# Optimization experiments

Measured on AMD Instinct MI355X. Metric: run time of the kernel, lower is better.

The kernel has to match this reference:

```python
import jax, jax.numpy as jnp
import numpy as np

B, S, D, H, DK, DFF = 4, 1024, 1024, 16, 64, 4096
EPS = 1e-5


def layer_norm(x, g, b):
    m = jnp.mean(x, axis=-1, keepdims=True)
    v = jnp.var(x, axis=-1, keepdims=True)
    return (x - m) * jax.lax.rsqrt(v + EPS) * g + b


def setup_inputs() -> dict:
    key = jax.random.key(0)
    ks = jax.random.split(key, 12)
    sc = 0.02
    return {
        "x":    jax.random.normal(ks[0], (B, S, D), jnp.float32),
        # per-head Q/K/V projections, stacked over heads: [H, D, DK]
        "Wq":   jax.random.normal(ks[1], (H, D, DK), jnp.float32) * sc,
        "bq":   jnp.zeros((H, DK), jnp.float32),
        "Wk":   jax.random.normal(ks[2], (H, D, DK), jnp.float32) * sc,
        "bk":   jnp.zeros((H, DK), jnp.float32),
        "Wv":   jax.random.normal(ks[3], (H, D, DK), jnp.float32) * sc,
        "bv":   jnp.zeros((H, DK), jnp.float32),
        # output projection: [H*DK, D]
        "Wo":   jax.random.normal(ks[4], (H * DK, D), jnp.float32) * sc,
        "bo":   jnp.zeros((D,), jnp.float32),
        # FFN
        "W1":   jax.random.normal(ks[5], (D, DFF), jnp.float32) * sc,
        "b1":   jnp.zeros((DFF,), jnp.float32),
        "W2":   jax.random.normal(ks[6], (DFF, D), jnp.float32) * sc,
        "b2":   jnp.zeros((D,), jnp.float32),
        # LayerNorms
        "g1":   jnp.ones((D,), jnp.float32),
        "be1":  jnp.zeros((D,), jnp.float32),
        "g2":   jnp.ones((D,), jnp.float32),
        "be2":  jnp.zeros((D,), jnp.float32),
    }


def reference(x, Wq, bq, Wk, bk, Wv, bv, Wo, bo, W1, b1, W2, b2, g1, be1, g2, be2):
    # batched multi-head attention (original loops per head; math identical)
    q = jnp.einsum("bsd,hdk->bhsk", x, Wq) + bq[None, :, None, :]
    k = jnp.einsum("bsd,hdk->bhsk", x, Wk) + bk[None, :, None, :]
    v = jnp.einsum("bsd,hdk->bhsk", x, Wv) + bv[None, :, None, :]
    scale = 1.0 / jnp.sqrt(jnp.asarray(DK, x.dtype))
    scores = jnp.einsum("bhsk,bhtk->bhst", q * scale, k)
    attn = jax.nn.softmax(scores, axis=-1)  # dropout = eval-mode identity
    o = jnp.einsum("bhst,bhtk->bhsk", attn, v)
    # torch.cat over heads along dim 2 -> [B, S, H*DK]
    o = jnp.transpose(o, (0, 2, 1, 3)).reshape(B, S, H * DK)
    att = o @ Wo + bo
    # post-attn: residual of LayerNorm(att)
    x = x + layer_norm(att, g1, be1)
    # FFN
    pos = jax.nn.relu(x @ W1 + b1) @ W2 + b2
    x = x + layer_norm(pos, g2, be2)
    return x
```

## Files before the change

### kernel.cpp

```cpp
#include <hip/hip_runtime.h>
#include <hip/hip_bf16.h>
#include <hip/hip_fp16.h>

typedef unsigned short u16;
typedef short bf16x8_t __attribute__((ext_vector_type(8)));
typedef float f32x4_t  __attribute__((ext_vector_type(4)));

__device__ __forceinline__ u16 f2bf(float f) {
    __hip_bfloat16 h = __float2bfloat16(f);
    union { __hip_bfloat16 b; u16 u; } cv; cv.b = h; return cv.u;
}

__device__ __forceinline__ void g2l16(const void* g, void* l) {
    __builtin_amdgcn_global_load_lds(
        (const __attribute__((address_space(1))) unsigned int*)g,
        (__attribute__((address_space(3))) unsigned int*)l, 16, 0, 0);
}

__global__ __launch_bounds__(256)
void k_prep(const float* __restrict__ x, u16* __restrict__ Xb,
            const float* __restrict__ Wq, const float* __restrict__ Wk,
            const float* __restrict__ Wv, u16* __restrict__ Wqkvt,
            const float* __restrict__ Wo, const float* __restrict__ W1,
            const float* __restrict__ W2, u16* __restrict__ Wot,
            u16* __restrict__ W1t, u16* __restrict__ W2t)
{
    int id = blockIdx.x;
    if (id < 4096) {
        int i = id * 256 + threadIdx.x;
        float4 f = ((const float4*)x)[i];
        ushort4 o;
        o.x = f2bf(f.x); o.y = f2bf(f.y); o.z = f2bf(f.z); o.w = f2bf(f.w);
        ((ushort4*)Xb)[i] = o;
        return;
    }
    id -= 4096;
    const float* in; u16* out; int R, C, r0, c0;
    if (id < 768) {
        int zx = id >> 8, hy = (id >> 4) & 15, tx = id & 15;
        in  = (zx == 0 ? Wq : (zx == 1 ? Wk : Wv)) + (size_t)hy * 65536;
        out = Wqkvt + ((size_t)zx * 1024 + hy * 64) * 1024;
        R = 1024; C = 64; r0 = tx * 64; c0 = 0;
    } else {
        id -= 768;
        int tx, ty;
        if (id < 256)       { in = Wo; out = Wot; R = 1024; C = 1024; tx = id & 15; ty = id >> 4; }
        else if (id < 1280) { id -= 256; in = W1; out = W1t; R = 1024; C = 4096; tx = id & 63; ty = id >> 6; }
        else                { id -= 1280; in = W2; out = W2t; R = 4096; C = 1024; tx = id & 15; ty = id >> 4; }
        r0 = ty * 64; c0 = tx * 64;
    }
    __shared__ float t[64][65];
    int lc = threadIdx.x & 63, lr = threadIdx.x >> 6;
#pragma unroll
    for (int p = 0; p < 16; ++p) {
        int rr = p * 4 + lr;
        t[rr][lc] = in[(size_t)(r0 + rr) * C + c0 + lc];
    }
    __syncthreads();
#pragma unroll
    for (int p = 0; p < 16; ++p) {
        int cc = p * 4 + lr;
        out[(size_t)(c0 + cc) * R + r0 + lc] = f2bf(t[lc][cc]);
    }
}

__global__ __launch_bounds__(256)
void k_vt(const u16* __restrict__ V, u16* __restrict__ VT) {
    __shared__ u16 t[64 * 72];
    int bh = blockIdx.y, s0 = blockIdx.x * 64;
    const u16* Vp = V + (size_t)bh * 65536;
    u16* Tp = VT + (size_t)bh * 65536;
    int tid = threadIdx.x;
    int r = tid >> 3, c = (tid & 7) * 8;
    *(uint4*)&t[r * 72 + c]        = *(const uint4*)&Vp[(size_t)(s0 + r) * 64 + c];
    *(uint4*)&t[(r + 32) * 72 + c] = *(const uint4*)&Vp[(size_t)(s0 + r + 32) * 64 + c];
    __syncthreads();
    int d = tid >> 2, sl0 = (tid & 3) * 16;
    uint4 outv[2];
    u16* ov = (u16*)outv;
#pragma unroll
    for (int j = 0; j < 16; ++j) ov[j] = t[(sl0 + j) * 72 + d];
    *(uint4*)&Tp[(size_t)d * 1024 + s0 + sl0]     = outv[0];
    *(uint4*)&Tp[(size_t)d * 1024 + s0 + sl0 + 8] = outv[1];
}

__global__ __launch_bounds__(256, 4)
void k_gemm_bt(const u16* __restrict__ A, const u16* __restrict__ Bt,
               void* __restrict__ out, int M, int N, int K, int kchunk)
{
    __shared__ __align__(16) u16 As[2 * 128 * 32];
    __shared__ __align__(16) u16 Bs[2 * 128 * 32];
    int tid = threadIdx.x;
    int wave = tid >> 6, lane = tid & 63;

    int nx = gridDim.x, nwg = nx * gridDim.y;
    int f  = blockIdx.x + nx * blockIdx.y;
    int f2 = (f & 7) * (nwg >> 3) + (f >> 3);
    int bx = f2 % nx, by = f2 / nx;
    int row0 = by * 128, col0 = bx * 128;

    int z = blockIdx.z;
    int kbeg = z * kchunk;

    int lrow = lane >> 2, lcol = (lane & 3) * 8;
    const u16* pA0 = A  + (size_t)(row0 + wave * 16 + lrow) * K + kbeg + lcol;
    const u16* pA1 = pA0 + (size_t)64 * K;
    const u16* pB0 = Bt + (size_t)(col0 + wave * 16 + lrow) * K + kbeg + lcol;
    const u16* pB1 = pB0 + (size_t)64 * K;
    u16* lA0 = &As[wave * 512];
    u16* lA1 = &As[2048 + wave * 512];
    u16* lB0 = &Bs[wave * 512];
    u16* lB1 = &Bs[2048 + wave * 512];

    int wm = (wave >> 1) * 64, wn = (wave & 1) * 64;
    int quad = lane >> 4, l16 = lane & 15;

    f32x4_t acc[4][4];
#pragma unroll
    for (int i = 0; i < 4; i++)
#pragma unroll
        for (int j = 0; j < 4; j++) acc[i][j] = f32x4_t{0.f, 0.f, 0.f, 0.f};

    for (int kk = 0; kk < kchunk; kk += 64) {
        __syncthreads();
        g2l16(pA0, lA0);      g2l16(pA1, lA1);
        g2l16(pA0 + 32, lA0 + 4096); g2l16(pA1 + 32, lA1 + 4096);
        g2l16(pB0, lB0);      g2l16(pB1, lB1);
        g2l16(pB0 + 32, lB0 + 4096); g2l16(pB1 + 32, lB1 + 4096);
        pA0 += 64; pA1 += 64; pB0 += 64; pB1 += 64;
        __syncthreads();

#pragma unroll
        for (int s = 0; s < 2; ++s) {
            const u16* as = &As[s * 4096];
            const u16* bs = &Bs[s * 4096];
            bf16x8_t a[4], b[4];
#pragma unroll
            for (int i = 0; i < 4; ++i)
                a[i] = *(const bf16x8_t*)&as[(wm + i * 16 + l16) * 32 + quad * 8];
#pragma unroll
            for (int j = 0; j < 4; ++j)
                b[j] = *(const bf16x8_t*)&bs[(wn + j * 16 + l16) * 32 + quad * 8];
#pragma unroll
            for (int i = 0; i < 4; ++i)
#pragma unroll
                for (int j = 0; j < 4; ++j)
                    acc[i][j] = __builtin_amdgcn_mfma_f32_16x16x32_bf16(a[i], b[j], acc[i][j], 0, 0, 0);
        }
    }

#pragma unroll
    for (int i = 0; i < 4; ++i)
#pragma unroll
        for (int j = 0; j < 4; ++j)
#pragma unroll
            for (int r = 0; r < 4; ++r) {
                int row = row0 + wm + i * 16 + quad * 4 + r;
                int col = col0 + wn + j * 16 + l16;
                ((__half*)out)[(size_t)z * M * N + (size_t)row * N + col] =
                    __float2half(acc[i][j][r]);
            }
}

template<int EPI>
__global__ __launch_bounds__(512, 4)
void k_gemm_bt2(const u16* __restrict__ A, const u16* __restrict__ Bt,
                const float* __restrict__ bias0, const float* __restrict__ bias1,
                const float* __restrict__ bias2, void* __restrict__ out,
                int M, int N, int K)
{
    __shared__ __align__(16) u16 As[2 * 256 * 32];
    __shared__ __align__(16) u16 Bs[2 * 128 * 32];
    int tid = threadIdx.x;
    int wave = tid >> 6, lane = tid & 63;
    int row0 = blockIdx.y * 256, col0 = blockIdx.x * 128;

    int lrow = lane >> 2, lcol = (lane & 3) * 8;
    const u16* pA0 = A  + (size_t)(row0 + wave * 16 + lrow) * K + lcol;
    const u16* pA1 = pA0 + (size_t)128 * K;
    const u16* pB0 = Bt + (size_t)(col0 + wave * 16 + lrow) * K + lcol;
    u16* lA0 = &As[wave * 512];
    u16* lA1 = &As[4096 + wave * 512];
    u16* lB0 = &Bs[wave * 512];

    int wm = (wave >> 1) * 64, wn = (wave & 1) * 64;
    int quad = lane >> 4, l16 = lane & 15;

    f32x4_t acc[4][4];
#pragma unroll
    for (int i = 0; i < 4; i++)
#pragma unroll
        for (int j = 0; j < 4; j++) acc[i][j] = f32x4_t{0.f, 0.f, 0.f, 0.f};

    for (int kk = 0; kk < K; kk += 64) {
        __syncthreads();
        g2l16(pA0, lA0);           g2l16(pA1, lA1);
        g2l16(pA0 + 32, lA0 + 8192); g2l16(pA1 + 32, lA1 + 8192);
        g2l16(pB0, lB0);           g2l16(pB0 + 32, lB0 + 4096);
        pA0 += 64; pA1 += 64; pB0 += 64;
        __syncthreads();

#pragma unroll
        for (int s = 0; s < 2; ++s) {
            const u16* as = &As[s * 8192];
            const u16* bs = &Bs[s * 4096];
            bf16x8_t a[4], b[4];
#pragma unroll
            for (int i = 0; i < 4; ++i)
                a[i] = *(const bf16x8_t*)&as[(wm + i * 16 + l16) * 32 + quad * 8];
#pragma unroll
            for (int j = 0; j < 4; ++j)
                b[j] = *(const bf16x8_t*)&bs[(wn + j * 16 + l16) * 32 + quad * 8];
#pragma unroll
            for (int i = 0; i < 4; ++i)
#pragma unroll
                for (int j = 0; j < 4; ++j)
                    acc[i][j] = __builtin_amdgcn_mfma_f32_16x16x32_bf16(a[i], b[j], acc[i][j], 0, 0, 0);
        }
    }

#pragma unroll
    for (int i = 0; i < 4; ++i)
#pragma unroll
        for (int j = 0; j < 4; ++j)
#pragma unroll
            for (int r = 0; r < 4; ++r) {
                int row = row0 + wm + i * 16 + quad * 4 + r;
                int col = col0 + wn + j * 16 + l16;
                float v = acc[i][j][r];
                if (EPI == 1) {
                    ((u16*)out)[(size_t)row * N + col] = f2bf(fmaxf(v + bias0[col], 0.f));
                } else {
                    int proj = col >> 10, within = col & 1023;
                    const float* bp = proj == 0 ? bias0 : (proj == 1 ? bias1 : bias2);
                    v += bp[within];
                    if (proj == 0) v *= 0.18033688f;
                    int h = within >> 6, kq = within & 63;
                    int b_ = row >> 10, s_ = row & 1023;
                    size_t bh = (size_t)((b_ << 4) + h);
                    ((u16*)out)[(size_t)proj * 4194304 + bh * 65536 + (s_ << 6) + kq] = f2bf(v);
                }
            }
}

__global__ __launch_bounds__(512, 4)
void k_attn(const u16* __restrict__ Qg, const u16* __restrict__ Kg,
            const u16* __restrict__ VTg, u16* __restrict__ Og)
{
    __shared__ __align__(16) u16 Ks[64 * 64];
    __shared__ __align__(16) u16 Vs[64 * 64];
    __shared__ __align__(16) u16 Ps[128 * 64];

    int tid = threadIdx.x, wave = tid >> 6, lane = tid & 63;
    int quad = lane >> 4, l16 = lane & 15;

    int f  = blockIdx.x + gridDim.x * blockIdx.y;
    int f2 = (f & 7) * ((gridDim.x * gridDim.y) >> 3) + (f >> 3);
    int bh = f2 >> 3;
    int q0 = (f2 & 7) * 128;
    int wrow = wave * 16;

    const u16* Qp  = Qg  + (size_t)bh * 65536;
    const u16* Kp  = Kg  + (size_t)bh * 65536;
    const u16* VTp = VTg + (size_t)bh * 65536;

    int arow_g = q0 + wrow + l16;
    bf16x8_t aq0 = *(const bf16x8_t*)&Qp[(size_t)arow_g * 64 + quad * 8];
    bf16x8_t aq1 = *(const bf16x8_t*)&Qp[(size_t)arow_g * 64 + 32 + quad * 8];

    int srow = tid >> 3, scb = tid & 7;
    uint4 kreg = *(const uint4*)&Kp[(size_t)srow * 64 + scb * 8];
    uint4 vreg = *(const uint4*)&VTp[(size_t)srow * 1024 + scb * 8];
    u16* kdst = &Ks[srow * 64 + ((scb ^ (srow & 7)) * 8)];
    u16* vdst = &Vs[srow * 64 + ((scb ^ (srow & 7)) * 8)];

    f32x4_t o[4], lsum;
#pragma unroll
    for (int nt = 0; nt < 4; ++nt) o[nt] = f32x4_t{0.f, 0.f, 0.f, 0.f};
    lsum = f32x4_t{0.f, 0.f, 0.f, 0.f};

    bf16x8_t ones;
#pragma unroll
    for (int j = 0; j < 8; ++j) ones[j] = (short)0x3F80;

    int a7 = l16 & 7;

    for (int kv0 = 0; kv0 < 1024; kv0 += 64) {
        __syncthreads();
        *(uint4*)kdst = kreg;
        *(uint4*)vdst = vreg;
        __syncthreads();
        if (kv0 < 960) {
            kreg = *(const uint4*)&Kp[(size_t)(kv0 + 64 + srow) * 64 + scb * 8];
            vreg = *(const uint4*)&VTp[(size_t)srow * 1024 + kv0 + 64 + scb * 8];
        }

        f32x4_t s[4];
#pragma unroll
        for (int nt = 0; nt < 4; ++nt) {
            int brow = nt * 16 + l16;
            bf16x8_t bk0 = *(const bf16x8_t*)&Ks[brow * 64 + ((quad ^ a7) * 8)];
            bf16x8_t bk1 = *(const bf16x8_t*)&Ks[brow * 64 + (((4 + quad) ^ a7) * 8)];
            s[nt] = __builtin_amdgcn_mfma_f32_16x16x32_bf16(aq0, bk0, f32x4_t{0.f,0.f,0.f,0.f}, 0, 0, 0);
            s[nt] = __builtin_amdgcn_mfma_f32_16x16x32_bf16(aq1, bk1, s[nt], 0, 0, 0);
        }

#pragma unroll
        for (int nt = 0; nt < 4; ++nt) {
            int pcb = nt * 2 + (l16 >> 3);
#pragma unroll
            for (int r = 0; r < 4; ++r) {
                float p = exp2f(s[nt][r]);
                int pr = wrow + quad * 4 + r;
                Ps[pr * 64 + ((pcb ^ (pr & 7)) * 8) + (l16 & 7)] = f2bf(p);
            }
        }

        int arow = wrow + l16;
        bf16x8_t ap0 = *(const bf16x8_t*)&Ps[arow * 64 + ((quad ^ a7) * 8)];
        bf16x8_t ap1 = *(const bf16x8_t*)&Ps[arow * 64 + (((4 + quad) ^ a7) * 8)];
#pragma unroll
        for (int nt = 0; nt < 4; ++nt) {
            int vrow = nt * 16 + l16;
            bf16x8_t bv0 = *(const bf16x8_t*)&Vs[vrow * 64 + ((quad ^ a7) * 8)];
            bf16x8_t bv1 = *(const bf16x8_t*)&Vs[vrow * 64 + (((4 + quad) ^ a7) * 8)];
            o[nt] = __builtin_amdgcn_mfma_f32_16x16x32_bf16(ap0, bv0, o[nt], 0, 0, 0);
            o[nt] = __builtin_amdgcn_mfma_f32_16x16x32_bf16(ap1, bv1, o[nt], 0, 0, 0);
        }
        lsum = __builtin_amdgcn_mfma_f32_16x16x32_bf16(ap0, ones, lsum, 0, 0, 0);
        lsum = __builtin_amdgcn_mfma_f32_16x16x32_bf16(ap1, ones, lsum, 0, 0, 0);
    }

    int b = bh >> 4, h = bh & 15;
    float invl[4];
#pragma unroll
    for (int r = 0; r < 4; ++r) invl[r] = 1.f / lsum[r];
#pragma unroll
    for (int nt = 0; nt < 4; ++nt)
#pragma unroll
        for (int r = 0; r < 4; ++r) {
            int srow2 = q0 + wrow + quad * 4 + r;
            Og[(size_t)(b * 1024 + srow2) * 1024 + (h << 6) + nt * 16 + l16] = f2bf(o[nt][r] * invl[r]);
        }
}

template<int MODE, int NP>
__global__ __launch_bounds__(256)
void k_ln2(const __half* __restrict__ p, const float* __restrict__ bias,
           const float* __restrict__ residf, const u16* __restrict__ residb,
           const float* __restrict__ g, const float* __restrict__ be,
           float* __restrict__ out, u16* __restrict__ outb)
{
    int row = blockIdx.x, tid = threadIdx.x;
    size_t base = (size_t)row * 1024;
    float xv[4]; float s = 0.f, sq = 0.f;
#pragma unroll
    for (int i = 0; i < 4; i++) {
        int c = tid + i * 256;
        float t = bias[c];
#pragma unroll
        for (int z = 0; z < NP; ++z) t += __half2float(p[(size_t)z * 4194304 + base + c]);
        xv[i] = t;
        s += t; sq += t * t;
    }
#pragma unroll
    for (int off = 32; off; off >>= 1) { s += __shfl_down(s, off); sq += __shfl_down(sq, off); }
    __shared__ float ss[4], ssq[4];
    int wv = tid >> 6;
    if ((tid & 63) == 0) { ss[wv] = s; ssq[wv] = sq; }
    __syncthreads();
    s  = ss[0] + ss[1] + ss[2] + ss[3];
    sq = ssq[0] + ssq[1] + ssq[2] + ssq[3];
    float mean = s * (1.f / 1024.f);
    float var  = sq * (1.f / 1024.f) - mean * mean;
    float rstd = rsqrtf(var + 1e-5f);
#pragma unroll
    for (int i = 0; i < 4; i++) {
        int c = tid + i * 256;
        float rv;
        if (MODE == 0) rv = residf[base + c];
        else {
            union { u16 u[2]; unsigned int w; float f; } cv;
            cv.w = (unsigned int)residb[base + c] << 16;
            rv = cv.f;
        }
        float y = rv + (xv[i] - mean) * rstd * g[c] + be[c];
        if (MODE == 0) outb[base + c] = f2bf(y);
        else           out[base + c] = y;
    }
}

extern "C" void kernel_launch(void* const* d_in, const int* in_sizes, int n_in,
                              void* d_out, int out_size, void* d_ws, size_t ws_size,
                              hipStream_t stream) {
    const float* x   = (const float*)d_in[0];
    const float* Wq  = (const float*)d_in[1];
    const float* bq  = (const float*)d_in[2];
    const float* Wk  = (const float*)d_in[3];
    const float* bk  = (const float*)d_in[4];
    const float* Wv  = (const float*)d_in[5];
    const float* bv  = (const float*)d_in[6];
    const float* Wo  = (const float*)d_in[7];
    const float* bo  = (const float*)d_in[8];
    const float* W1  = (const float*)d_in[9];
    const float* b1  = (const float*)d_in[10];
    const float* W2  = (const float*)d_in[11];
    const float* b2  = (const float*)d_in[12];
    const float* g1  = (const float*)d_in[13];
    const float* be1 = (const float*)d_in[14];
    const float* g2  = (const float*)d_in[15];
    const float* be2 = (const float*)d_in[16];
    float* out = (float*)d_out;

    char* w = (char*)d_ws;
    u16*    Xb    = (u16*)(w);
    u16*    VTb   = (u16*)(w);
    u16*    Wqkvt = (u16*)(w + 8388608);
    u16*    Wot   = (u16*)(w + 14680064);
    u16*    W1t   = (u16*)(w + 16777216);
    u16*    W2t   = (u16*)(w + 25165824);
    u16*    Qb    = (u16*)(w + 33554432);
    u16*    Kb    = (u16*)(w + 41943040);
    u16*    Vb    = (u16*)(w + 50331648);
    u16*    Oc    = (u16*)(w + 58720256);
    __half* part4 = (__half*)(w + 33554432);
    __half* part2 = (__half*)(w + 67108864);
    u16*    x1b   = (u16*)(w + 117440512);
    u16*    hb    = (u16*)(w + 125829120);

    k_prep<<<7168, 256, 0, stream>>>(x, Xb, Wq, Wk, Wv, Wqkvt, Wo, W1, W2, Wot, W1t, W2t);

    k_gemm_bt2<2><<<dim3(24, 16), 512, 0, stream>>>(Xb, Wqkvt, bq, bk, bv, Qb, 4096, 3072, 1024);

    k_vt<<<dim3(16, 64), 256, 0, stream>>>(Vb, VTb);

    k_attn<<<dim3(8, 64), 512, 0, stream>>>(Qb, Kb, VTb, Oc);

    k_gemm_bt<<<dim3(8, 32, 2), 256, 0, stream>>>(Oc, Wot, part2, 4096, 1024, 1024, 512);

    k_ln2<0, 2><<<4096, 256, 0, stream>>>(part2, bo, x, nullptr, g1, be1, nullptr, x1b);

    k_gemm_bt2<1><<<dim3(32, 16), 512, 0, stream>>>(x1b, W1t, b1, nullptr, nullptr, hb, 4096, 4096, 1024);

    k_gemm_bt<<<dim3(8, 32, 4), 256, 0, stream>>>(hb, W2t, part4, 4096, 1024, 4096, 1024);

    k_ln2<1, 4><<<4096, 256, 0, stream>>>(part4, b2, nullptr, x1b, g2, be2, out, nullptr);
}
```

Measured before the change: 308.4 us.

## Add 256x256-tile ping-pong GEMM kernel for both FFN matmuls

Introduces a new bf16 MFMA GEMM with 256x256 block tiles, 8 waves each computing 128x64, double-buffered LDS filled by direct global-to-LDS loads, and interleaved quarter-tile MFMA phases with setprio and barriers to overlap loads with compute. It replaces the previous kernels for the W1 (bias+ReLU epilogue) and W2 (split-K fp16 partials) FFN GEMMs. The aim is more data reuse per LDS load and better overlap of memory traffic with math. In exchange it uses 128KB of LDS per block and launches fewer workgroups, which lowers occupancy and leaves fewer blocks to spread across the CUs.

```diff
diff --git a/kernel.cpp b/kernel.cpp
--- a/kernel.cpp
+++ b/kernel.cpp
@@ -239,6 +239,151 @@
                     int b_ = row >> 10, s_ = row & 1023;
                     size_t bh = (size_t)((b_ << 4) + h);
                     ((u16*)out)[(size_t)proj * 4194304 + bh * 65536 + (s_ << 6) + kq] = f2bf(v);
+                }
+            }
+}
+
+template<int EPI>
+__global__ __launch_bounds__(512, 2)
+void k_gemm8p(const u16* __restrict__ A, const u16* __restrict__ Bt,
+              const float* __restrict__ bias0, void* __restrict__ out,
+              int M, int N, int K, int kchunk)
+{
+    __shared__ __align__(16) u16 As[2][16384];
+    __shared__ __align__(16) u16 Bs[2][16384];
+
+    const int tid = threadIdx.x;
+    const int wave = tid >> 6, lane = tid & 63;
+    const int quad = lane >> 4, l16 = lane & 15;
+    const int wm = (wave >> 2) * 128;
+    const int wn = (wave & 3) * 64;
+
+    int nx = gridDim.x, nwg = nx * gridDim.y;
+    int f  = blockIdx.x + nx * blockIdx.y;
+    int f2 = (f & 7) * (nwg >> 3) + (f >> 3);
+    int row0 = (f2 / nx) * 256, col0 = (f2 % nx) * 256;
+    int z = blockIdx.z, kbeg = z * kchunk;
+    int nk = kchunk >> 6;
+
+    const int rr0 = tid >> 3, cg = tid & 7;
+    const int xc = (cg ^ (rr0 & 7)) * 8;
+    const u16* Ag = A  + (size_t)(row0 + rr0) * K + kbeg + xc;
+    const u16* Bg = Bt + (size_t)(col0 + rr0) * K + kbeg + xc;
+    const int ldst = tid * 8;
+
+#define STA(bsel, h, kt) do { \
+    const u16* _s = Ag + (size_t)(h) * 128 * K + (size_t)(kt) * 64; \
+    g2l16(_s, &As[bsel][(h) * 8192 + ldst]); \
+    g2l16(_s + (size_t)64 * K, &As[bsel][(h) * 8192 + 4096 + ldst]); } while (0)
+#define STB(bsel, h, kt) do { \
+    const u16* _s = Bg + (size_t)(h) * 128 * K + (size_t)(kt) * 64; \
+    g2l16(_s, &Bs[bsel][(h) * 8192 + ldst]); \
+    g2l16(_s + (size_t)64 * K, &Bs[bsel][(h) * 8192 + 4096 + ldst]); } while (0)
+
+#define RDA(b, mi, ks) (*(const bf16x8_t*)&As[b][(wm + (mi) * 16 + l16) * 64 + ((((ks) * 4 + quad) ^ (l16 & 7)) * 8)])
+#define RDB(b, nj, ks) (*(const bf16x8_t*)&Bs[b][(wn + (nj) * 16 + l16) * 64 + ((((ks) * 4 + quad) ^ (l16 & 7)) * 8)])
+
+    f32x4_t acc[8][4];
+#pragma unroll
+    for (int i = 0; i < 8; ++i)
+#pragma unroll
+        for (int j = 0; j < 4; ++j) acc[i][j] = f32x4_t{0.f, 0.f, 0.f, 0.f};
+
+    bf16x8_t av0[4][2], av1[4][2], bv0[2][2], bv1[2][2];
+
+    STA(0, 0, 0); STA(0, 1, 0); STB(0, 0, 0); STB(0, 1, 0);
+    if (nk > 1) {
+        STB(1, 0, 1);
+        asm volatile("s_waitcnt vmcnt(2)" ::: "memory");
+    } else {
+        asm volatile("s_waitcnt vmcnt(0)" ::: "memory");
+    }
+    __builtin_amdgcn_s_barrier();
+#pragma unroll
+    for (int i = 0; i < 4; ++i) { av0[i][0] = RDA(0, i, 0); av0[i][1] = RDA(0, i, 1); }
+#pragma unroll
+    for (int j = 0; j < 2; ++j) { bv0[j][0] = RDB(0, j, 0); bv0[j][1] = RDB(0, j, 1); }
+    __builtin_amdgcn_sched_barrier(0);
+
+    for (int t = 0; t < nk; ++t) {
+        int b = t & 1, bn = b ^ 1;
+        if (t + 1 < nk) STB(bn, 1, t + 1);
+#pragma unroll
+        for (int j = 0; j < 2; ++j) { bv1[j][0] = RDB(b, 2 + j, 0); bv1[j][1] = RDB(b, 2 + j, 1); }
+        __builtin_amdgcn_sched_barrier(0);
+        __builtin_amdgcn_s_setprio(1);
+#pragma unroll
+        for (int i = 0; i < 4; ++i)
+#pragma unroll
+            for (int j = 0; j < 2; ++j) {
+                acc[i][j] = __builtin_amdgcn_mfma_f32_16x16x32_bf16(av0[i][0], bv0[j][0], acc[i][j], 0, 0, 0);
+                acc[i][j] = __builtin_amdgcn_mfma_f32_16x16x32_bf16(av0[i][1], bv0[j][1], acc[i][j], 0, 0, 0);
+            }
+        __builtin_amdgcn_s_setprio(0);
+        __builtin_amdgcn_s_barrier();
+        if (t + 1 < nk) { STA(bn, 0, t + 1); STA(bn, 1, t + 1); }
+#pragma unroll
+        for (int i = 0; i < 4; ++i) { av1[i][0] = RDA(b, 4 + i, 0); av1[i][1] = RDA(b, 4 + i, 1); }
+        __builtin_amdgcn_sched_barrier(0);
+        __builtin_amdgcn_s_setprio(1);
+#pragma unroll
+        for (int i = 0; i < 4; ++i)
+#pragma unroll
+            for (int j = 0; j < 2; ++j) {
+                acc[i][2 + j] = __builtin_amdgcn_mfma_f32_16x16x32_bf16(av0[i][0], bv1[j][0], acc[i][2 + j], 0, 0, 0);
+                acc[i][2 + j] = __builtin_amdgcn_mfma_f32_16x16x32_bf16(av0[i][1], bv1[j][1], acc[i][2 + j], 0, 0, 0);
+            }
+        __builtin_amdgcn_s_setprio(0);
+        __builtin_amdgcn_s_barrier();
+        __builtin_amdgcn_s_setprio(1);
+#pragma unroll
+        for (int i = 0; i < 4; ++i)
+#pragma unroll
+            for (int j = 0; j < 2; ++j) {
+                acc[4 + i][j] = __builtin_amdgcn_mfma_f32_16x16x32_bf16(av1[i][0], bv0[j][0], acc[4 + i][j], 0, 0, 0);
+                acc[4 + i][j] = __builtin_amdgcn_mfma_f32_16x16x32_bf16(av1[i][1], bv0[j][1], acc[4 + i][j], 0, 0, 0);
+            }
+        __builtin_amdgcn_s_setprio(0);
+        __builtin_amdgcn_s_barrier();
+        asm volatile("s_waitcnt vmcnt(0)" ::: "memory");
+        if (t + 2 < nk) STB(b, 0, t + 2);
+        __builtin_amdgcn_s_barrier();
+        if (t + 1 < nk) {
+#pragma unroll
+            for (int i = 0; i < 4; ++i) { av0[i][0] = RDA(bn, i, 0); av0[i][1] = RDA(bn, i, 1); }
+#pragma unroll
+            for (int j = 0; j < 2; ++j) { bv0[j][0] = RDB(bn, j, 0); bv0[j][1] = RDB(bn, j, 1); }
+            __builtin_amdgcn_sched_barrier(0);
+        }
+        __builtin_amdgcn_s_setprio(1);
+#pragma unroll
+        for (int i = 0; i < 4; ++i)
+#pragma unroll
+            for (int j = 0; j < 2; ++j) {
+                acc[4 + i][2 + j] = __builtin_amdgcn_mfma_f32_16x16x32_bf16(av1[i][0], bv1[j][0], acc[4 + i][2 + j], 0, 0, 0);
+                acc[4 + i][2 + j] = __builtin_amdgcn_mfma_f32_16x16x32_bf16(av1[i][1], bv1[j][1], acc[4 + i][2 + j], 0, 0, 0);
+            }
+        __builtin_amdgcn_s_setprio(0);
+        __builtin_amdgcn_s_barrier();
+    }
+#undef STA
+#undef STB
+#undef RDA
+#undef RDB
+
+#pragma unroll
+    for (int mi = 0; mi < 8; ++mi)
+#pragma unroll
+        for (int nj = 0; nj < 4; ++nj)
+#pragma unroll
+            for (int r = 0; r < 4; ++r) {
+                int row = row0 + wm + mi * 16 + quad * 4 + r;
+                int col = col0 + wn + nj * 16 + l16;
+                float v = acc[mi][nj][r];
+                if (EPI == 0) {
+                    ((__half*)out)[(size_t)z * M * N + (size_t)row * N + col] = __float2half(v);
+                } else {
+                    ((u16*)out)[(size_t)row * N + col] = f2bf(fmaxf(v + bias0[col], 0.f));
                 }
             }
 }
@@ -440,9 +585,9 @@
 
     k_ln2<0, 2><<<4096, 256, 0, stream>>>(part2, bo, x, nullptr, g1, be1, nullptr, x1b);
 
-    k_gemm_bt2<1><<<dim3(32, 16), 512, 0, stream>>>(x1b, W1t, b1, nullptr, nullptr, hb, 4096, 4096, 1024);
-
-    k_gemm_bt<<<dim3(8, 32, 4), 256, 0, stream>>>(hb, W2t, part4, 4096, 1024, 4096, 1024);
+    k_gemm8p<1><<<dim3(16, 16), 512, 0, stream>>>(x1b, W1t, b1, hb, 4096, 4096, 1024, 1024);
+
+    k_gemm8p<0><<<dim3(4, 16, 4), 512, 0, stream>>>(hb, W2t, nullptr, part4, 4096, 1024, 4096, 1024);
 
     k_ln2<1, 4><<<4096, 256, 0, stream>>>(part4, b2, nullptr, x1b, g2, be2, out, nullptr);
 }
```

Measured after the change: 331.8 us. 1.08x slower.
